# Optimization experiments

Measured on AMD Instinct MI355X. Metric: run time of the kernel, lower is better.

The kernel has to match this reference:

```python
import jax, jax.numpy as jnp
import numpy as np
from jax import lax

DN = ('NCHW', 'OIHW', 'NCHW')

def conv(x, w, groups=1):
    return lax.conv_general_dilated(x, w, (1, 1), 'SAME',
                                    feature_group_count=groups,
                                    dimension_numbers=DN)

def layernorm_cf(x, w, b, eps=1e-6):
    # channels-first LayerNorm over dim=1
    u = x.mean(1, keepdims=True)
    s = ((x - u) ** 2).mean(1, keepdims=True)
    xn = (x - u) / jnp.sqrt(s + eps)
    return w[None, :, None, None] * xn + b[None, :, None, None]

def l2norm(x, eps=1e-12):
    n = jnp.sqrt(jnp.sum(x * x, axis=-1, keepdims=True))
    return x / jnp.maximum(n, eps)

def setup_inputs() -> dict:
    key = jax.random.key(0)
    ks = jax.random.split(key, 16)
    B, C, H, W = 4, 192, 128, 128
    heads = 6
    hidden = int(C * 2.66)  # 510
    s = 0.02
    rn = lambda k, shp: jax.random.normal(k, shp, dtype=jnp.float32) * s
    return {
        'x': jax.random.normal(ks[0], (B, C, H, W), dtype=jnp.float32),
        'ln_w': jnp.ones((C,), jnp.float32),
        'ln_b': jnp.zeros((C,), jnp.float32),
        'temperature': jnp.ones((heads, 1, 1), jnp.float32),
        'q_w': rn(ks[1], (C, C, 1, 1)),
        'q_dw_w': rn(ks[2], (C, 1, 3, 3)),
        'kv_w': rn(ks[3], (2 * C, C, 1, 1)),
        'kv_dw_w': rn(ks[4], (2 * C, 1, 3, 3)),
        'proj_w': rn(ks[5], (C, C, 1, 1)),
        'pos_embed': rn(ks[6], (1, C, 1, 1)),
        'pos_q_w': rn(ks[7], (C, C, 1, 1)),
        'pos_k_w': rn(ks[8], (C, C, 1, 1)),
        'sel_in_w': rn(ks[9], (hidden, C, 3, 3)),
        'sel_dw_w': rn(ks[10], (hidden, 1, 3, 3)),
        'sel_out_w': rn(ks[11], (C, hidden, 3, 3)),
        'alpha': jnp.float32(0.5),
    }

def reference(x, ln_w, ln_b, temperature, q_w, q_dw_w, kv_w, kv_dw_w,
              proj_w, pos_embed, pos_q_w, pos_k_w,
              sel_in_w, sel_dw_w, sel_out_w, alpha):
    b, c, h, w = x.shape
    heads = temperature.shape[0]
    ch = c // heads
    n = h * w

    # --- CFA on norm_x (norm_x == norm_y since both are norm(x)) ---
    norm_x = layernorm_cf(x, ln_w, ln_b)
    q = conv(conv(norm_x, q_w), q_dw_w, groups=c)
    kv = conv(conv(norm_x, kv_w), kv_dw_w, groups=2 * c)
    k, v = jnp.split(kv, 2, axis=1)

    q = q.reshape(b, heads, ch, n)
    k = k.reshape(b, heads, ch, n)
    v = v.reshape(b, heads, ch, n)

    qn = l2norm(q)
    kn = l2norm(k)
    attn = jax.nn.softmax(jnp.einsum('bhcn,bhdn->bhcd', qn, kn) * temperature[None], axis=-1)
    out = jnp.einsum('bhcd,bhdn->bhcn', attn, v)

    pos_x = norm_x + pos_embed
    pos_q = conv(pos_x, pos_q_w).reshape(b, heads, ch, n)
    pos_k = conv(pos_x, pos_k_w).reshape(b, heads, ch, n)
    pos_attn = jax.nn.softmax(jnp.einsum('bhcn,bhdn->bhcd', pos_q, pos_k), axis=-1)
    pos_out = jnp.einsum('bhcd,bhdn->bhcn', pos_attn, v)

    out = (out + pos_out).reshape(b, c, h, w)
    out = conv(out, proj_w)
    x = x + alpha * out

    # --- SEL (conv-FFN) ---
    nx = layernorm_cf(x, ln_w, ln_b)
    g = conv(nx, sel_in_w)
    g = conv(g, sel_dw_w, groups=g.shape[1])
    g = jax.nn.silu(g)
    g = conv(g, sel_out_w)
    x = x + (1.0 - alpha) * g
    return x
```

## Files before the change

### kernel.cpp

```cpp
#include <hip/hip_runtime.h>
#include <hip/hip_bf16.h>
#include <stdint.h>

#define DEVI __device__ __forceinline__

typedef __attribute__((ext_vector_type(8))) unsigned short us8;
typedef __attribute__((ext_vector_type(8))) __bf16 bf16x8;
typedef __attribute__((ext_vector_type(4))) float f32x4;

#define BB 4
#define CC 192
#define HH 128
#define NPIX 16384
#define MTOT 65536
#define HEADS 6

DEVI float b2f(unsigned short u){ return __uint_as_float(((unsigned)u)<<16); }
DEVI unsigned short f2b(float f){
  unsigned u = __float_as_uint(f);
  return (unsigned short)((u + 0x7fffu + ((u>>16)&1u)) >> 16);
}

DEVI void gload16(const void* g, void* l){
  __builtin_amdgcn_global_load_lds((const __attribute__((address_space(1))) unsigned int*)g,
                                   (__attribute__((address_space(3))) unsigned int*)l,
                                   16, 0, 0);
}

__global__ __launch_bounds__(256)
void ln1_k(const float* __restrict__ x, const float* __restrict__ lnw,
           const float* __restrict__ lnb, unsigned short* __restrict__ nx)
{
  __shared__ float tile[CC*65];
  __shared__ float stats[64*2];
  int gbase = blockIdx.x * 64;
  int b = gbase >> 14; int n0 = gbase & (NPIX-1);
  for (int idx = threadIdx.x; idx < CC*64; idx += 256){
    int c = idx >> 6, j = idx & 63;
    tile[c*65 + j] = x[((size_t)b*CC + c)*NPIX + n0 + j];
  }
  __syncthreads();
  if (threadIdx.x < 64){
    int j = threadIdx.x;
    float s = 0.f, ss = 0.f;
    for (int c = 0; c < CC; c++){ float v = tile[c*65 + j]; s += v; ss += v*v; }
    float mu = s * (1.f/CC);
    float var = ss * (1.f/CC) - mu*mu;
    stats[j*2] = mu; stats[j*2+1] = rsqrtf(var + 1e-6f);
  }
  __syncthreads();
  for (int idx = threadIdx.x; idx < CC*64; idx += 256){
    int c = idx % CC, j = idx / CC;
    float v = (tile[c*65 + j] - stats[j*2]) * stats[j*2+1] * lnw[c] + lnb[c];
    nx[(size_t)(gbase + j)*CC + c] = f2b(v);
  }
}

__global__ __launch_bounds__(256)
void ln2_k(const float* __restrict__ x2, const float* __restrict__ lnw,
           const float* __restrict__ lnb, unsigned short* __restrict__ nx)
{
  int gm = blockIdx.x*4 + (threadIdx.x >> 6);
  int lane = threadIdx.x & 63;
  const float* row = x2 + (size_t)gm*CC;
  float v0 = row[lane], v1 = row[lane+64], v2 = row[lane+128];
  float s = v0+v1+v2, ss = v0*v0+v1*v1+v2*v2;
  #pragma unroll
  for (int o = 32; o >= 1; o >>= 1){
    s  += __shfl_xor(s,  o);
    ss += __shfl_xor(ss, o);
  }
  float mu = s * (1.f/CC);
  float rstd = rsqrtf(ss*(1.f/CC) - mu*mu + 1e-6f);
  unsigned short* o0 = nx + (size_t)gm*CC;
  o0[lane]     = f2b((v0-mu)*rstd*lnw[lane]     + lnb[lane]);
  o0[lane+64]  = f2b((v1-mu)*rstd*lnw[lane+64]  + lnb[lane+64]);
  o0[lane+128] = f2b((v2-mu)*rstd*lnw[lane+128] + lnb[lane+128]);
}

template<int EPI, int NSLICES>
__global__ __launch_bounds__(256, 2)
void gemm_k(const unsigned short* __restrict__ A, int strideA,
            const unsigned short* __restrict__ W, int Ktot, int sliceC,
            int NcolsW, int NcolsStore, int outStride, int colBlocks,
            unsigned short* __restrict__ outB,
            const float* __restrict__ bias,
            const float* __restrict__ res,
            float* __restrict__ outF,
            const float* __restrict__ alphaP,
            const unsigned short* __restrict__ zerop)
{
  __shared__ unsigned short lds[2*128*64];
  unsigned short* ldsA = lds;
  unsigned short* ldsB = lds + 128*64;

  const int tid = threadIdx.x;
  const int lane = tid & 63;
  const int wv = tid >> 6;
  const int q8 = gridDim.x >> 3;
  const int bid = (blockIdx.x & 7)*q8 + (blockIdx.x >> 3);
  const int mblk = bid / colBlocks;
  const int nblk = bid - mblk*colBlocks;
  const int m0 = mblk*128, co0 = nblk*128;

  const int jT = lane & 7;
  int rowT[4];
  #pragma unroll
  for (int i = 0; i < 4; i++) rowT[i] = ((wv*4 + i)*64 + lane) >> 3;

  const unsigned short* bsrc[4];
  #pragma unroll
  for (int i = 0; i < 4; i++){
    int co = co0 + rowT[i];
    int jj = jT ^ (rowT[i] & 7);
    bsrc[i] = (co < NcolsW) ? (W + (size_t)co*Ktot + (jj << 3))
                            : (zerop + (lane << 3));
  }

  const unsigned short* asrc[4];
  int gmA[4], jjA[4];
  #pragma unroll
  for (int i = 0; i < 4; i++){
    gmA[i] = m0 + rowT[i];
    jjA[i] = jT ^ (rowT[i] & 7);
    asrc[i] = A + (size_t)gmA[i]*strideA + (jjA[i] << 3);
  }

  f32x4 acc[4][4] = {};
  int ci0 = 0, s = 0, dy = -1, dx = -1;

  for (int k0 = 0; k0 < Ktot; k0 += 64){
    if constexpr (NSLICES == 1){
      #pragma unroll
      for (int i = 0; i < 4; i++){
        gload16(asrc[i], (char*)ldsA + (wv*4 + i)*1024);
        asrc[i] += 64;
      }
    } else {
      #pragma unroll
      for (int i = 0; i < 4; i++){
        int gm = gmA[i];
        int np = gm & (NPIX-1);
        int hh = np >> 7, ww = np & 127;
        int h2 = hh + dy, w2 = ww + dx;
        const unsigned short* src = ((unsigned)h2 < 128u && (unsigned)w2 < 128u)
          ? (A + (size_t)(gm + dy*HH + dx)*strideA + ci0 + (jjA[i] << 3))
          : (zerop + (lane << 3));
        gload16(src, (char*)ldsA + (wv*4 + i)*1024);
      }
    }
    #pragma unroll
    for (int i = 0; i < 4; i++){
      gload16(bsrc[i], (char*)ldsB + (wv*4 + i)*1024);
      bsrc[i] += 64;
    }
    asm volatile("s_waitcnt vmcnt(0)" ::: "memory");
    __syncthreads();

    #pragma unroll
    for (int kk = 0; kk < 2; kk++){
      bf16x8 af[4], bfr[4];
      int kb = kk*64 + ((lane >> 4) << 4);
      #pragma unroll
      for (int mi = 0; mi < 4; mi++){
        int rm = (wv >> 1)*64 + mi*16 + (lane & 15);
        int off = rm*128 + (kb ^ ((rm & 7) << 4));
        af[mi] = *(const bf16x8*)((const char*)ldsA + off);
      }
      #pragma unroll
      for (int ni = 0; ni < 4; ni++){
        int rb = (wv & 1)*64 + ni*16 + (lane & 15);
        int off = rb*128 + (kb ^ ((rb & 7) << 4));
        bfr[ni] = *(const bf16x8*)((const char*)ldsB + off);
      }
      #pragma unroll
      for (int mi = 0; mi < 4; mi++)
        #pragma unroll
        for (int ni = 0; ni < 4; ni++)
          acc[mi][ni] = __builtin_amdgcn_mfma_f32_16x16x32_bf16(af[mi], bfr[ni], acc[mi][ni], 0, 0, 0);
    }
    __syncthreads();

    if constexpr (NSLICES > 1){
      s++; if (s == 9){ s = 0; ci0 += 64; }
      dy = s/3 - 1; dx = s - (s/3)*3 - 1;
    }
  }
  (void)sliceC;

  float alpha = 0.f;
  if (EPI == 1) alpha = *alphaP;
  if (EPI == 2) alpha = 1.f - *alphaP;
  const int colb = co0 + (wv & 1)*64;
  const int rowb = m0 + (wv >> 1)*64;
  #pragma unroll
  for (int mi = 0; mi < 4; mi++){
    int r0 = rowb + mi*16 + ((lane >> 4) << 2);
    #pragma unroll
    for (int ni = 0; ni < 4; ni++){
      int co = colb + ni*16 + (lane & 15);
      if (co < NcolsStore){
        float bv = (EPI == 0 && bias) ? bias[co] : 0.f;
        #pragma unroll
        for (int r = 0; r < 4; r++){
          int gm = r0 + r;
          float v = acc[mi][ni][r];
          if constexpr (EPI == 0){
            outB[(size_t)gm*outStride + co] = f2b(v + bv);
          } else if constexpr (EPI == 1){
            int b = gm >> 14, np = gm & (NPIX-1);
            outF[(size_t)gm*CC + co] = res[((size_t)b*CC + co)*NPIX + np] + alpha*v;
          } else {
            int b = gm >> 14, np = gm & (NPIX-1);
            outF[((size_t)b*CC + co)*NPIX + np] = res[(size_t)gm*CC + co] + alpha*v;
          }
        }
      }
    }
  }
}

template<int NCHV, int DOSILU>
__global__ __launch_bounds__(256)
void dw_k(const unsigned short* __restrict__ src, int strideS,
          const float* __restrict__ wtT, int wstride,
          unsigned short* __restrict__ dst, int strideD)
{
  const int q8 = gridDim.x >> 3;
  const int bid = (blockIdx.x & 7)*q8 + (blockIdx.x >> 3);
  int idx = bid*256 + threadIdx.x;
  int gm = idx / NCHV;
  int cb = idx - gm*NCHV;
  int c = cb*8;
  int np = gm & (NPIX-1);
  int hh = np >> 7, ww = np & 127;
  float acc[8] = {0,0,0,0,0,0,0,0};
  #pragma unroll
  for (int s = 0; s < 9; s++){
    int dy = s/3 - 1, dx = s%3 - 1;
    int h2 = hh + dy, w2 = ww + dx;
    if ((unsigned)h2 < 128u && (unsigned)w2 < 128u){
      us8 t = *(const us8*)(src + (size_t)(gm + dy*HH + dx)*strideS + c);
      f32x4 w0 = *(const f32x4*)(wtT + s*wstride + c);
      f32x4 w1 = *(const f32x4*)(wtT + s*wstride + c + 4);
      #pragma unroll
      for (int j = 0; j < 4; j++){
        acc[j]   += b2f(t[j])   * w0[j];
        acc[4+j] += b2f(t[4+j]) * w1[j];
      }
    }
  }
  us8 o;
  #pragma unroll
  for (int j = 0; j < 8; j++){
    float v = acc[j];
    if (DOSILU) v = v / (1.f + __expf(-v));
    o[j] = f2b(v);
  }
  *(us8*)(dst + (size_t)gm*strideD + c) = o;
}

__global__ __launch_bounds__(192)
void sumsq_k(const unsigned short* __restrict__ q, int stride, float* __restrict__ part)
{
  int b = blockIdx.x >> 5, ch = blockIdx.x & 31;
  int c = threadIdx.x;
  const unsigned short* base = q + ((size_t)b*NPIX + ch*512)*stride + c;
  float acc = 0.f;
  for (int r = 0; r < 512; r++){ float v = b2f(base[(size_t)r*stride]); acc += v*v; }
  part[(size_t)(b*32 + ch)*CC + c] = acc;
}

__global__ __launch_bounds__(256)
void pairdot_k(const unsigned short* __restrict__ qb, const unsigned short* __restrict__ kb,
               int stride, float* __restrict__ Spart)
{
  __shared__ float qs[32][129];
  __shared__ float ks[32][129];
  int bh = blockIdx.x >> 3;
  int chunk = blockIdx.x & 7;
  int b = bh / HEADS, h = bh - b*HEADS;
  int t = threadIdx.x;
  int cP = t >> 3;
  int dg = t & 7;
  size_t gm0 = (size_t)b*NPIX + chunk*2048;
  int r = t >> 1, hf = t & 1;
  float acc0=0, acc1=0, acc2=0, acc3=0;
  for (int sub = 0; sub < 16; sub++){
    __syncthreads();
    {
      const unsigned short* pq = qb + (gm0 + sub*128 + r)*stride + h*32 + hf*16;
      const unsigned short* pk = kb + (gm0 + sub*128 + r)*stride + h*32 + hf*16;
      us8 a0 = *(const us8*)pq; us8 a1 = *(const us8*)(pq + 8);
      us8 b0 = *(const us8*)pk; us8 b1 = *(const us8*)(pk + 8);
      #pragma unroll
      for (int j = 0; j < 8; j++){
        qs[hf*16 + j][r]     = b2f(a0[j]);
        qs[hf*16 + 8 + j][r] = b2f(a1[j]);
        ks[hf*16 + j][r]     = b2f(b0[j]);
        ks[hf*16 + 8 + j][r] = b2f(b1[j]);
      }
    }
    __syncthreads();
    for (int n = 0; n < 128; n++){
      float qv = qs[cP][n];
      acc0 += qv * ks[dg*4+0][n];
      acc1 += qv * ks[dg*4+1][n];
      acc2 += qv * ks[dg*4+2][n];
      acc3 += qv * ks[dg*4+3][n];
    }
  }
  float* o = Spart + (size_t)blockIdx.x*1024 + cP*32 + dg*4;
  o[0]=acc0; o[1]=acc1; o[2]=acc2; o[3]=acc3;
}

__global__ __launch_bounds__(64)
void smax_k(const float* __restrict__ Spos, const float* __restrict__ Scfa,
            const float* __restrict__ qnp, const float* __restrict__ knp,
            const float* __restrict__ temp, float* __restrict__ att)
{
  int bh = blockIdx.x; int b = bh / HEADS, h = bh - b*HEADS;
  __shared__ float kn[32];
  int t = threadIdx.x;
  if (t < 32){
    float ss = 0.f;
    for (int ck = 0; ck < 32; ck++) ss += knp[((size_t)b*32 + ck)*CC + h*32 + t];
    kn[t] = fmaxf(sqrtf(ss), 1e-12f);
  }
  __syncthreads();
  if (t >= 32) return;
  int c = t;
  float ssq = 0.f;
  for (int ck = 0; ck < 32; ck++) ssq += qnp[((size_t)b*32 + ck)*CC + h*32 + c];
  float qn = fmaxf(sqrtf(ssq), 1e-12f);
  float rowS[32], rowP[32];
  #pragma unroll
  for (int d = 0; d < 32; d++){
    float sv = 0.f, pv = 0.f;
    for (int ck = 0; ck < 8; ck++){
      sv += Scfa[(size_t)(bh*8 + ck)*1024 + c*32 + d];
      pv += Spos[(size_t)(bh*8 + ck)*1024 + c*32 + d];
    }
    rowS[d] = sv; rowP[d] = pv;
  }
  float tv = temp[h];
  float m1 = -3e38f, m2 = -3e38f;
  #pragma unroll
  for (int d = 0; d < 32; d++){
    rowS[d] = rowS[d] / (qn*kn[d]) * tv;
    m1 = fmaxf(m1, rowS[d]);
    m2 = fmaxf(m2, rowP[d]);
  }
  float s1 = 0.f, s2 = 0.f;
  #pragma unroll
  for (int d = 0; d < 32; d++){
    rowS[d] = __expf(rowS[d] - m1); s1 += rowS[d];
    rowP[d] = __expf(rowP[d] - m2); s2 += rowP[d];
  }
  float r1 = 1.f/s1, r2 = 1.f/s2;
  #pragma unroll
  for (int d = 0; d < 32; d++)
    att[(size_t)bh*1024 + c*32 + d] = rowS[d]*r1 + rowP[d]*r2;
}

__global__ __launch_bounds__(256)
void pv_k(const float* __restrict__ att, const unsigned short* __restrict__ vd, int stride,
          unsigned short* __restrict__ outT)
{
  __shared__ float As[32][33];
  int bh = blockIdx.x >> 8; int mc = blockIdx.x & 255;
  int b = bh / HEADS, h = bh - b*HEADS;
  int t = threadIdx.x;
  for (int i = t; i < 1024; i += 256) As[i >> 5][i & 31] = att[(size_t)bh*1024 + i];
  __syncthreads();
  int gm = b*NPIX + mc*64 + (t >> 2);
  int cq = t & 3;
  const unsigned short* vp = vd + (size_t)gm*stride + h*32;
  float acc[8] = {0,0,0,0,0,0,0,0};
  for (int d = 0; d < 32; d++){
    float vv = b2f(vp[d]);
    #pragma unroll
    for (int j = 0; j < 8; j++) acc[j] += As[cq*8 + j][d] * vv;
  }
  us8 o;
  #pragma unroll
  for (int j = 0; j < 8; j++) o[j] = f2b(acc[j]);
  *(us8*)(outT + (size_t)gm*CC + h*32 + cq*8) = o;
}

__global__ void castcopy_k(const float* __restrict__ s, unsigned short* __restrict__ d, int n){
  int i = blockIdx.x*256 + threadIdx.x; if (i < n) d[i] = f2b(s[i]);
}
__global__ void prepselin_k(const float* __restrict__ s, unsigned short* __restrict__ d){
  int i = blockIdx.x*256 + threadIdx.x;
  if (i >= 510*1728) return;
  int co = i / 1728, rem = i - co*1728;
  int chunk = rem >> 6, e = rem & 63;
  int cib = chunk / 9, sl = chunk - cib*9;
  int ci = cib*64 + e;
  d[i] = f2b(s[(size_t)(co*192 + ci)*9 + sl]);
}
__global__ void prepselout_k(const float* __restrict__ s, unsigned short* __restrict__ d){
  int i = blockIdx.x*256 + threadIdx.x;
  if (i >= 192*4608) return;
  int co = i / 4608, rem = i - co*4608;
  int chunk = rem >> 6, e = rem & 63;
  int cib = chunk / 9, sl = chunk - cib*9;
  int ci = cib*64 + e;
  d[i] = (ci < 510) ? f2b(s[(size_t)(co*510 + ci)*9 + sl]) : (unsigned short)0;
}
__global__ void prepbias_k(const float* __restrict__ pq, const float* __restrict__ pk,
                           const float* __restrict__ pe, float* __restrict__ bias){
  int r = blockIdx.x*64 + threadIdx.x;
  if (r >= 960) return;
  float s = 0.f;
  if (r < 384){
    const float* Wp = (r < 192) ? pq : pk;
    int co = (r < 192) ? r : r - 192;
    for (int ci = 0; ci < 192; ci++) s += Wp[co*192 + ci]*pe[ci];
  }
  bias[r] = s;
}
__global__ void prepdwT_k(const float* __restrict__ qdw, const float* __restrict__ kvdw,
                          const float* __restrict__ seldw,
                          float* __restrict__ wqkv, float* __restrict__ wsel){
  int i = blockIdx.x*256 + threadIdx.x;
  if (i < 9*576){
    int s = i / 576, c = i - s*576;
    wqkv[i] = (c < 192) ? qdw[c*9 + s] : kvdw[(size_t)(c-192)*9 + s];
  }
  int j = i - 9*576;
  if (j >= 0 && j < 9*512){
    int s = j / 512, c = j - s*512;
    wsel[j] = (c < 510) ? seldw[(size_t)c*9 + s] : 0.f;
  }
}

extern "C" void kernel_launch(void* const* d_in, const int* in_sizes, int n_in,
                              void* d_out, int out_size, void* d_ws, size_t ws_size,
                              hipStream_t stream)
{
  const float* x       = (const float*)d_in[0];
  const float* ln_w    = (const float*)d_in[1];
  const float* ln_b    = (const float*)d_in[2];
  const float* temp    = (const float*)d_in[3];
  const float* q_w     = (const float*)d_in[4];
  const float* q_dw    = (const float*)d_in[5];
  const float* kv_w    = (const float*)d_in[6];
  const float* kv_dw   = (const float*)d_in[7];
  const float* proj_w  = (const float*)d_in[8];
  const float* pos_e   = (const float*)d_in[9];
  const float* posq_w  = (const float*)d_in[10];
  const float* posk_w  = (const float*)d_in[11];
  const float* selin_w = (const float*)d_in[12];
  const float* seldw_w = (const float*)d_in[13];
  const float* selout_w= (const float*)d_in[14];
  const float* alphaP  = (const float*)d_in[15];

  char* ws = (char*)d_ws;
  unsigned short* zerop  = (unsigned short*)(ws + 0);
  float* biasC           = (float*)(ws + 4096);
  float* Spos            = (float*)(ws + 8192);
  float* Scfa            = (float*)(ws + 794624);
  float* qnp             = (float*)(ws + 1581056);
  float* knp             = (float*)(ws + 1679360);
  float* att             = (float*)(ws + 1777664);
  unsigned short* WC     = (unsigned short*)(ws + 2097152);
  unsigned short* Wproj  = (unsigned short*)(ws + 2465792);
  unsigned short* Wselin = (unsigned short*)(ws + 2539520);
  unsigned short* Wselout= (unsigned short*)(ws + 4302080);
  float* WdwQKV          = (float*)(ws + 6071552);
  float* WdwSEL          = (float*)(ws + 6092288);
  unsigned short* normx  = (unsigned short*)(ws + 8388608);
  unsigned short* outT   = normx;
  unsigned short* qp     = (unsigned short*)(ws + 33554432);
  float*          x2     = (float*)(ws + 33554432);
  unsigned short* nx     = (unsigned short*)(ws + 83886080);
  unsigned short* g2     = (unsigned short*)(ws + 83886080);
  unsigned short* qkvd   = (unsigned short*)(ws + 159383552);
  unsigned short* g      = qkvd;

  hipMemsetAsync(zerop, 0, 4096, stream);

  castcopy_k<<<144, 256, 0, stream>>>(posq_w, WC,          36864);
  castcopy_k<<<144, 256, 0, stream>>>(posk_w, WC + 36864,  36864);
  castcopy_k<<<144, 256, 0, stream>>>(q_w,    WC + 73728,  36864);
  castcopy_k<<<288, 256, 0, stream>>>(kv_w,   WC + 110592, 73728);
  castcopy_k<<<144, 256, 0, stream>>>(proj_w, Wproj,       36864);
  prepselin_k<<<3443, 256, 0, stream>>>(selin_w, Wselin);
  prepselout_k<<<3456, 256, 0, stream>>>(selout_w, Wselout);
  prepbias_k<<<15, 64, 0, stream>>>(posq_w, posk_w, pos_e, biasC);
  prepdwT_k<<<39, 256, 0, stream>>>(q_dw, kv_dw, seldw_w, WdwQKV, WdwSEL);

  ln1_k<<<1024, 256, 0, stream>>>(x, ln_w, ln_b, normx);
  gemm_k<0,1><<<512*8, 256, 0, stream>>>(normx, 192, WC, 192, 192, 960, 960, 960, 8,
                                         qp, biasC, nullptr, nullptr, nullptr, zerop);
  pairdot_k<<<192, 256, 0, stream>>>(qp, qp + 192, 960, Spos);
  dw_k<72,0><<<18432, 256, 0, stream>>>(qp + 384, 960, WdwQKV, 576, qkvd, 576);
  sumsq_k<<<128, 192, 0, stream>>>(qkvd,       576, qnp);
  sumsq_k<<<128, 192, 0, stream>>>(qkvd + 192, 576, knp);
  pairdot_k<<<192, 256, 0, stream>>>(qkvd, qkvd + 192, 576, Scfa);
  smax_k<<<24, 64, 0, stream>>>(Spos, Scfa, qnp, knp, temp, att);
  pv_k<<<24*256, 256, 0, stream>>>(att, qkvd + 384, 576, outT);
  gemm_k<1,1><<<512*2, 256, 0, stream>>>(outT, 192, Wproj, 192, 192, 192, 192, 0, 2,
                                         nullptr, nullptr, x, x2, alphaP, zerop);
  ln2_k<<<16384, 256, 0, stream>>>(x2, ln_w, ln_b, nx);
  gemm_k<0,9><<<512*4, 256, 0, stream>>>(nx, 192, Wselin, 1728, 192, 510, 512, 512, 4,
                                         g, nullptr, nullptr, nullptr, nullptr, zerop);
  dw_k<64,1><<<16384, 256, 0, stream>>>(g, 512, WdwSEL, 512, g2, 512);
  gemm_k<2,9><<<512*2, 256, 0, stream>>>(g2, 512, Wselout, 4608, 512, 192, 192, 0, 2,
                                         nullptr, nullptr, x2, (float*)d_out, alphaP, zerop);
}
```

Before: 939.6 us.

## Use 256x256-tile GEMM kernel for SEL 3x3 implicit-GEMM convolutions

```diff
diff --git a/kernel.cpp b/kernel.cpp
--- a/kernel.cpp
+++ b/kernel.cpp
@@ -76,6 +76,140 @@
   o0[lane]     = f2b((v0-mu)*rstd*lnw[lane]     + lnb[lane]);
   o0[lane+64]  = f2b((v1-mu)*rstd*lnw[lane+64]  + lnb[lane+64]);
   o0[lane+128] = f2b((v2-mu)*rstd*lnw[lane+128] + lnb[lane+128]);
+}
+
+template<int EPI, int NSLICES>
+__global__ __launch_bounds__(512, 2)
+void gemm256_k(const unsigned short* __restrict__ A, int strideA,
+               const unsigned short* __restrict__ W, int Ktot,
+               int NcolsW, int NcolsStore, int outStride, int colBlocks,
+               unsigned short* __restrict__ outB,
+               const float* __restrict__ res, float* __restrict__ outF,
+               const float* __restrict__ alphaP,
+               const unsigned short* __restrict__ zerop)
+{
+  __shared__ unsigned short lds[65536];
+
+  const int tid = threadIdx.x;
+  const int l  = tid & 63;
+  const int w  = tid >> 6;
+  const int wm = w >> 2;
+  const int wn = w & 3;
+
+  const int q8 = gridDim.x >> 3;
+  const int bid = (blockIdx.x & 7)*q8 + (blockIdx.x >> 3);
+  const int mblk = bid / colBlocks;
+  const int nblk = bid - mblk*colBlocks;
+  const int m0 = mblk*256, co0 = nblk*256;
+
+  int rowT[4], slotX[4];
+  #pragma unroll
+  for (int i = 0; i < 4; i++){
+    rowT[i]  = (w*4 + i)*8 + (l >> 3);
+    slotX[i] = (l & 7) ^ (rowT[i] & 7);
+  }
+  const unsigned short* baseA[4];
+  int hhA[4], wwA[4];
+  #pragma unroll
+  for (int i = 0; i < 4; i++){
+    int gm = m0 + rowT[i];
+    int np = gm & (NPIX-1);
+    hhA[i] = np >> 7; wwA[i] = np & 127;
+    baseA[i] = A + (size_t)gm*strideA + (slotX[i] << 3);
+  }
+  const unsigned short* baseB[4];
+  bool bval[4];
+  #pragma unroll
+  for (int i = 0; i < 4; i++){
+    int co = co0 + rowT[i];
+    bval[i] = (co < NcolsW);
+    baseB[i] = bval[i] ? (W + (size_t)co*Ktot + (slotX[i] << 3)) : (zerop + (l << 3));
+  }
+
+  const int NT = Ktot >> 6;
+
+  auto STAGE = [&](int ts){
+    int buf = ts & 1;
+    unsigned short* la = lds + buf*16384;
+    unsigned short* lb = lds + 32768 + buf*16384;
+    int ci0, dy = 0, dx = 0;
+    if constexpr (NSLICES == 1){ ci0 = ts << 6; }
+    else { int cib = ts/9, s = ts - cib*9; ci0 = cib << 6; dy = s/3 - 1; dx = s - (s/3)*3 - 1; }
+    #pragma unroll
+    for (int i = 0; i < 4; i++){
+      const unsigned short* srcA;
+      if constexpr (NSLICES == 1){
+        srcA = baseA[i] + ci0;
+      } else {
+        int h2 = hhA[i] + dy, w2 = wwA[i] + dx;
+        srcA = ((unsigned)h2 < 128u && (unsigned)w2 < 128u)
+             ? (baseA[i] + (dy*HH + dx)*strideA + ci0)
+             : (zerop + (l << 3));
+      }
+      gload16(srcA, la + (w*4 + i)*512);
+    }
+    #pragma unroll
+    for (int i = 0; i < 4; i++){
+      const unsigned short* srcB = bval[i] ? (baseB[i] + (ts << 6)) : baseB[i];
+      gload16(srcB, lb + (w*4 + i)*512);
+    }
+  };
+
+  f32x4 acc[8][4] = {};
+
+  STAGE(0);
+  asm volatile("s_waitcnt vmcnt(0)" ::: "memory");
+  __syncthreads();
+
+  for (int t = 0; t < NT; ++t){
+    if (t + 1 < NT) STAGE(t + 1);
+    const unsigned short* la = lds + (t & 1)*16384;
+    const unsigned short* lb = lds + 32768 + (t & 1)*16384;
+    __builtin_amdgcn_s_setprio(1);
+    #pragma unroll
+    for (int kk = 0; kk < 2; kk++){
+      int ks = kk*4 + (l >> 4);
+      bf16x8 bf[4];
+      #pragma unroll
+      for (int nf = 0; nf < 4; nf++){
+        int rb = wn*64 + nf*16 + (l & 15);
+        bf[nf] = *(const bf16x8*)(lb + rb*64 + ((ks ^ (rb & 7)) << 3));
+      }
+      #pragma unroll
+      for (int mf = 0; mf < 8; mf++){
+        int rm = wm*128 + mf*16 + (l & 15);
+        bf16x8 af = *(const bf16x8*)(la + rm*64 + ((ks ^ (rm & 7)) << 3));
+        #pragma unroll
+        for (int nf = 0; nf < 4; nf++)
+          acc[mf][nf] = __builtin_amdgcn_mfma_f32_16x16x32_bf16(af, bf[nf], acc[mf][nf], 0, 0, 0);
+      }
+    }
+    __builtin_amdgcn_s_setprio(0);
+    __syncthreads();
+  }
+
+  float alpha = (EPI == 2) ? (1.f - *alphaP) : 0.f;
+  #pragma unroll
+  for (int mf = 0; mf < 8; mf++){
+    int r0 = m0 + wm*128 + mf*16 + ((l >> 4) << 2);
+    #pragma unroll
+    for (int nf = 0; nf < 4; nf++){
+      int co = co0 + wn*64 + nf*16 + (l & 15);
+      if (co < NcolsStore){
+        #pragma unroll
+        for (int r = 0; r < 4; r++){
+          int gm = r0 + r;
+          float v = acc[mf][nf][r];
+          if constexpr (EPI == 0){
+            outB[(size_t)gm*outStride + co] = f2b(v);
+          } else {
+            int b = gm >> 14, np = gm & (NPIX-1);
+            outF[((size_t)b*CC + co)*NPIX + np] = res[(size_t)gm*CC + co] + alpha*v;
+          }
+        }
+      }
+    }
+  }
 }
 
 template<int EPI, int NSLICES>
@@ -505,9 +639,9 @@
   gemm_k<1,1><<<512*2, 256, 0, stream>>>(outT, 192, Wproj, 192, 192, 192, 192, 0, 2,
                                          nullptr, nullptr, x, x2, alphaP, zerop);
   ln2_k<<<16384, 256, 0, stream>>>(x2, ln_w, ln_b, nx);
-  gemm_k<0,9><<<512*4, 256, 0, stream>>>(nx, 192, Wselin, 1728, 192, 510, 512, 512, 4,
-                                         g, nullptr, nullptr, nullptr, nullptr, zerop);
+  gemm256_k<0,9><<<512, 512, 0, stream>>>(nx, 192, Wselin, 1728, 510, 512, 512, 2,
+                                          g, nullptr, nullptr, alphaP, zerop);
   dw_k<64,1><<<16384, 256, 0, stream>>>(g, 512, WdwSEL, 512, g2, 512);
-  gemm_k<2,9><<<512*2, 256, 0, stream>>>(g2, 512, Wselout, 4608, 512, 192, 192, 0, 2,
-                                         nullptr, nullptr, x2, (float*)d_out, alphaP, zerop);
-}
+  gemm256_k<2,9><<<256, 512, 0, stream>>>(g2, 512, Wselout, 4608, 192, 192, 0, 1,
+                                          nullptr, x2, (float*)d_out, alphaP, zerop);
+}
```

Result: faster. 878.5 us (-6.5%).
